# Kernel tuning notes

Measured on AMD Instinct MI355X. Metric: run time of the kernel, lower is better.

The kernel has to match this reference:

```python
import jax, jax.numpy as jnp
import numpy as np

D_MODEL = 256
NHEAD = 8
NLAYERS = 4
B, L, K = 8, 4096, 10
EPS_ATT = 1e-6
EPS_LN = 1e-5
EPS_COS = 1e-8


def setup_inputs() -> dict:
    key = jax.random.key(0)
    ks = jax.random.split(key, 12)
    s = 1.0 / np.sqrt(D_MODEL)
    s2 = 1.0 / np.sqrt(2 * D_MODEL)
    return {
        "ClassNum": K,
        "feat": jax.random.normal(ks[0], (B, L, D_MODEL), jnp.float32),
        "feat_class": jax.random.normal(ks[1], (B, K, D_MODEL), jnp.float32),
        "Wq": jax.random.normal(ks[2], (NLAYERS, D_MODEL, D_MODEL), jnp.float32) * s,
        "Wk": jax.random.normal(ks[3], (NLAYERS, D_MODEL, D_MODEL), jnp.float32) * s,
        "Wv": jax.random.normal(ks[4], (NLAYERS, D_MODEL, D_MODEL), jnp.float32) * s,
        "Wm": jax.random.normal(ks[5], (NLAYERS, D_MODEL, D_MODEL), jnp.float32) * s,
        "W1": jax.random.normal(ks[6], (NLAYERS, 2 * D_MODEL, 2 * D_MODEL), jnp.float32) * s2,
        "W2": jax.random.normal(ks[7], (NLAYERS, 2 * D_MODEL, D_MODEL), jnp.float32) * s2,
        "g1": jnp.ones((NLAYERS, D_MODEL), jnp.float32),
        "b1": jnp.zeros((NLAYERS, D_MODEL), jnp.float32),
        "g2": jnp.ones((NLAYERS, D_MODEL), jnp.float32),
        "b2": jnp.zeros((NLAYERS, D_MODEL), jnp.float32),
    }


def _layernorm(x, g, b):
    mu = jnp.mean(x, axis=-1, keepdims=True)
    xc = x - mu
    var = jnp.mean(xc * xc, axis=-1, keepdims=True)
    return g * xc * jax.lax.rsqrt(var + EPS_LN) + b


def _encoder_layer(x, oh, Wq, Wk, Wv, Wm, W1, W2, g1, b1, g2, b2):
    # x: [B,L,C], oh: [B,L,K] one-hot cluster assignment.
    # Per-cluster LoFTR linear self-attention via segment sums (exact: the
    # per-cluster v_length scaling in LinearAttention cancels algebraically).
    bsz, seq, cdim = x.shape
    hd = cdim // NHEAD
    q = (x @ Wq).reshape(bsz, seq, NHEAD, hd)
    k = (x @ Wk).reshape(bsz, seq, NHEAD, hd)
    v = (x @ Wv).reshape(bsz, seq, NHEAD, hd)
    Q = jax.nn.elu(q) + 1.0
    Kf = jax.nn.elu(k) + 1.0
    # per-(batch,cluster) sums: KV [B,K,H,D,D], Ksum [B,K,H,D]
    KV = jnp.einsum('blc,blhd,blhe->bchde', oh, Kf, v)
    Ksum = jnp.einsum('blc,blhd->bchd', oh, Kf)
    Kt = jnp.einsum('blc,bchd->blhd', oh, Ksum)  # cluster ΣK gathered per token
    Z = 1.0 / (jnp.einsum('blhd,blhd->blh', Q, Kt) + EPS_ATT)
    msg = jnp.zeros((bsz, seq, NHEAD, hd), x.dtype)
    for c in range(oh.shape[-1]):  # small fixed ClassNum loop
        msg = msg + oh[:, :, c][:, :, None, None] * jnp.einsum(
            'blhd,bhde->blhe', Q, KV[:, c])
    msg = msg * Z[..., None]
    m = msg.reshape(bsz, seq, cdim) @ Wm
    m = _layernorm(m, g1, b1)
    h = jnp.concatenate([x, m], axis=-1) @ W1
    h = jax.nn.relu(h) @ W2
    m = _layernorm(h, g2, b2)
    return x + m


def reference(ClassNum, feat, feat_class, Wq, Wk, Wv, Wm, W1, W2, g1, b1, g2, b2):
    x = jax.lax.stop_gradient(feat)          # feat.clone().detach()
    fc = jax.lax.stop_gradient(feat_class)   # feat_class.clone().detach()
    # cosine-similarity top-1 cluster routing (torch.F.cosine_similarity, eps=1e-8)
    na = jnp.linalg.norm(fc, axis=-1)  # [B,K]
    nb = jnp.linalg.norm(x, axis=-1)   # [B,L]
    dot = jnp.einsum('bkc,blc->bkl', fc, x)
    sim = dot / jnp.maximum(na[:, :, None] * nb[:, None, :], EPS_COS)
    seg = jnp.argmax(sim, axis=1)  # [B,L] cluster id per token
    oh = jax.nn.one_hot(seg, ClassNum, dtype=x.dtype)
    for li in range(Wq.shape[0]):
        x = _encoder_layer(x, oh, Wq[li], Wk[li], Wv[li], Wm[li],
                           W1[li], W2[li], g1[li], b1[li], g2[li], b2[li])
    return x
```

## Files before the change

kernel.cpp:

```cpp
#include <hip/hip_runtime.h>
#include <hip/hip_bf16.h>
#include <math.h>

#define DM 256
#define NHEAD 8
#define HD 32
#define NL 4
#define BATCH 8
#define SEQ 4096
#define KCLS 10
#define M_TOK (BATCH*SEQ)

#define BKG 64

#define PADPOS 5120
#define NWIN (PADPOS/64)
#define KVWIN 20
#define NGRP (KVWIN*4)

using bf16x8 = __attribute__((ext_vector_type(8))) short;
using f32x4  = __attribute__((ext_vector_type(4))) float;

__device__ __forceinline__ unsigned short f2bf(float f) {
    __hip_bfloat16 b = __float2bfloat16(f);
    return __builtin_bit_cast(unsigned short, b);
}
__device__ __forceinline__ float bf2f(unsigned short u) {
    unsigned v = (unsigned)u << 16;
    return __builtin_bit_cast(float, v);
}

__device__ __forceinline__ float wave_reduce_sum(float v) {
    #pragma unroll
    for (int off = 32; off > 0; off >>= 1) v += __shfl_xor(v, off, 64);
    return v;
}

__global__ __launch_bounds__(64) void fcn_kernel(const float* __restrict__ fc,
                                                 float* __restrict__ fcn) {
    int bk = blockIdx.x;
    int lane = threadIdx.x;
    float4 fv = *(const float4*)(fc + (size_t)bk * DM + lane * 4);
    float n = fv.x*fv.x + fv.y*fv.y + fv.z*fv.z + fv.w*fv.w;
    n = wave_reduce_sum(n);
    if (lane == 0) fcn[bk] = sqrtf(n);
}

__global__ void route_kernel(const float* __restrict__ feat, const float* __restrict__ fc,
                             const float* __restrict__ fcn,
                             float* __restrict__ x, unsigned short* __restrict__ xm,
                             int* __restrict__ seg) {
    int wid = (int)((blockIdx.x * (size_t)blockDim.x + threadIdx.x) >> 6);
    int lane = threadIdx.x & 63;
    if (wid >= M_TOK) return;
    int b = wid / SEQ;
    float4 xv = *(const float4*)(feat + (size_t)wid * DM + lane * 4);
    *(float4*)(x + (size_t)wid * DM + lane * 4) = xv;
    ushort4 u; u.x = f2bf(xv.x); u.y = f2bf(xv.y); u.z = f2bf(xv.z); u.w = f2bf(xv.w);
    *(ushort4*)(xm + (size_t)wid * 512 + lane * 4) = u;
    float nb2 = xv.x*xv.x + xv.y*xv.y + xv.z*xv.z + xv.w*xv.w;
    nb2 = wave_reduce_sum(nb2);
    float nb = sqrtf(nb2);
    float best = -1e30f; int bestk = 0;
    for (int k = 0; k < KCLS; ++k) {
        float4 fv = *(const float4*)(fc + ((size_t)(b * KCLS + k)) * DM + lane * 4);
        float d = fv.x*xv.x + fv.y*xv.y + fv.z*xv.z + fv.w*xv.w;
        d = wave_reduce_sum(d);
        float sim = d / fmaxf(fcn[b * KCLS + k] * nb, 1e-8f);
        if (sim > best) { best = sim; bestk = k; }
    }
    if (lane == 0) seg[wid] = bestk;
}

__global__ __launch_bounds__(256) void seg_count(const int* __restrict__ seg,
                                                 int* __restrict__ cnt) {
    __shared__ int wc[4][KCLS];
    int b = blockIdx.x >> 4, chunk = blockIdx.x & 15;
    int t = threadIdx.x, w = t >> 6, lane = t & 63;
    int c = seg[b * SEQ + chunk * 256 + t];
    #pragma unroll
    for (int cc = 0; cc < KCLS; ++cc) {
        unsigned long long m = __ballot(c == cc);
        if (lane == 0) wc[w][cc] = __popcll(m);
    }
    __syncthreads();
    if (t < KCLS)
        cnt[(b * 16 + chunk) * KCLS + t] = wc[0][t] + wc[1][t] + wc[2][t] + wc[3][t];
}

__global__ __launch_bounds__(256) void seg_scan(const int* __restrict__ cnt,
                                                int* __restrict__ chunkbase,
                                                int* __restrict__ wseg,
                                                int* __restrict__ psegp,
                                                int* __restrict__ grange) {
    __shared__ int sTot[BATCH][KCLS];
    __shared__ int sBase[BATCH][KCLS];
    int tid = threadIdx.x;
    if (tid < BATCH * KCLS) {
        int b = tid / KCLS, c = tid % KCLS;
        int run = 0;
        #pragma unroll
        for (int j = 0; j < 16; ++j) run += cnt[(b * 16 + j) * KCLS + c];
        sTot[b][c] = run;
    }
    __syncthreads();
    if (tid < BATCH) {
        int b = tid, pb = 0;
        for (int c = 0; c < KCLS; ++c) {
            sBase[b][c] = pb;
            int psz = (sTot[b][c] + 63) & ~63;
            grange[(b * KCLS + c) * 2]     = pb >> 6;
            grange[(b * KCLS + c) * 2 + 1] = (pb + psz) >> 6;
            int w0 = pb >> 6, w1 = (pb + psz) >> 6;
            for (int w = w0; w < w1; ++w) wseg[b * NWIN + w] = c;
            pb += psz;
        }
        for (int w = pb >> 6; w < NWIN; ++w) wseg[b * NWIN + w] = -1;
    }
    __syncthreads();
    for (int i = tid; i < BATCH * PADPOS; i += 256) {
        int b = i / PADPOS, pos = i % PADPOS;
        int c = KCLS - 1;
        #pragma unroll
        for (int cc = KCLS - 1; cc >= 1; --cc)
            if (pos < sBase[b][cc]) c = cc - 1;
        psegp[i] = c;
    }
    if (tid < BATCH * KCLS) {
        int b = tid / KCLS, c = tid % KCLS;
        int pre = 0;
        #pragma unroll
        for (int j = 0; j < 16; ++j) {
            chunkbase[(b * 16 + j) * KCLS + c] = sBase[b][c] + pre;
            pre += cnt[(b * 16 + j) * KCLS + c];
        }
    }
}

__global__ __launch_bounds__(256) void seg_scatter(const int* __restrict__ seg,
                                                   const int* __restrict__ chunkbase,
                                                   int* __restrict__ pidxp,
                                                   int* __restrict__ sortposG) {
    __shared__ int wc[4][KCLS];
    int b = blockIdx.x >> 4, chunk = blockIdx.x & 15;
    int t = threadIdx.x, w = t >> 6, lane = t & 63;
    int l = chunk * 256 + t;
    int c = seg[b * SEQ + l];
    int rank_w = 0;
    #pragma unroll
    for (int cc = 0; cc < KCLS; ++cc) {
        unsigned long long m = __ballot(c == cc);
        if (lane == 0) wc[w][cc] = __popcll(m);
        if (cc == c) rank_w = __popcll(m & ((1ULL << lane) - 1ULL));
    }
    __syncthreads();
    int rank = rank_w;
    for (int wp = 0; wp < 4; ++wp)
        if (wp < w) rank += wc[wp][c];
    int pos = chunkbase[(b * 16 + chunk) * KCLS + c] + rank;
    pidxp[b * PADPOS + pos] = l;
    sortposG[b * SEQ + l] = b * PADPOS + pos;
}

__global__ __launch_bounds__(256) void zero_pads(const int* __restrict__ pidxp,
                                                 unsigned short* __restrict__ Kb,
                                                 unsigned short* __restrict__ Vb) {
    int row = blockIdx.x * 8 + (threadIdx.x >> 5);
    int c8 = (threadIdx.x & 31) * 8;
    if (pidxp[row] >= 0) return;
    bf16x8 z = (bf16x8){0,0,0,0,0,0,0,0};
    *(bf16x8*)(Kb + (size_t)row * DM + c8) = z;
    *(bf16x8*)(Vb + (size_t)row * DM + c8) = z;
}

__global__ __launch_bounds__(256) void transpose_all(
    const float* __restrict__ Wq, const float* __restrict__ Wk,
    const float* __restrict__ Wv, const float* __restrict__ Wm,
    const float* __restrict__ W1, const float* __restrict__ W2,
    unsigned short* __restrict__ WqkvT, unsigned short* __restrict__ WmT,
    unsigned short* __restrict__ W1T, unsigned short* __restrict__ W2T)
{
    __shared__ float s[64][65];
    int bid = blockIdx.x;
    int li = bid / 160, r = bid % 160;
    const float* src; unsigned short* dst; int K, N, kx, ny;
    if (r < 64) {
        int which = r >> 4, idx = r & 15;
        K = 256; N = 256; kx = idx & 3; ny = idx >> 2;
        if (which == 0)      { src = Wq + (size_t)li*65536; dst = WqkvT + (size_t)li*768*256; }
        else if (which == 1) { src = Wk + (size_t)li*65536; dst = WqkvT + (size_t)li*768*256 + 65536; }
        else if (which == 2) { src = Wv + (size_t)li*65536; dst = WqkvT + (size_t)li*768*256 + 131072; }
        else                 { src = Wm + (size_t)li*65536; dst = WmT + (size_t)li*65536; }
    } else if (r < 128) {
        int idx = r - 64;
        K = 512; N = 512; kx = idx & 7; ny = idx >> 3;
        src = W1 + (size_t)li*262144; dst = W1T + (size_t)li*262144;
    } else {
        int idx = r - 128;
        K = 512; N = 256; kx = idx & 7; ny = idx >> 3;
        src = W2 + (size_t)li*131072; dst = W2T + (size_t)li*131072;
    }
    int k0 = kx * 64, n0 = ny * 64;
    int t = threadIdx.x;
    int rr = t >> 4, c4 = (t & 15) * 4;
    #pragma unroll
    for (int i = 0; i < 4; ++i) {
        float4 v = *(const float4*)(src + (size_t)(k0 + rr + i*16) * N + n0 + c4);
        s[c4+0][rr+i*16] = v.x; s[c4+1][rr+i*16] = v.y;
        s[c4+2][rr+i*16] = v.z; s[c4+3][rr+i*16] = v.w;
    }
    __syncthreads();
    #pragma unroll
    for (int i = 0; i < 4; ++i) {
        int nr = rr + i*16;
        ushort4 u;
        u.x = f2bf(s[nr][c4+0]); u.y = f2bf(s[nr][c4+1]);
        u.z = f2bf(s[nr][c4+2]); u.w = f2bf(s[nr][c4+3]);
        *(ushort4*)(dst + (size_t)(n0 + nr) * K + k0 + c4) = u;
    }
}

template<int KD, int AS, int MODE>
__global__ __launch_bounds__(512, 4) void mfma_gemm(
    const unsigned short* __restrict__ A, const unsigned short* __restrict__ Bt,
    const int* __restrict__ sortpos,
    unsigned short* __restrict__ Ob0, unsigned short* __restrict__ Ob1,
    unsigned short* __restrict__ Ob2)
{
    __shared__ unsigned short As[128 * BKG];
    __shared__ unsigned short Bs[256 * BKG];
    __shared__ int sPos[128];
    int t = threadIdx.x;
    int lane = t & 63;
    int w = t >> 6;
    int wm = w & 1, wn = w >> 1;
    int li = lane & 15, lg = lane >> 4;
    int bm = blockIdx.x * 128;
    int bn = blockIdx.y * 256;

    if (MODE == 1 && t < 128) sPos[t] = sortpos[bm + t];

    f32x4 acc[4][4];
    #pragma unroll
    for (int m = 0; m < 4; ++m)
        #pragma unroll
        for (int n = 0; n < 4; ++n)
            acc[m][n] = (f32x4){0.f, 0.f, 0.f, 0.f};

    for (int k0 = 0; k0 < KD; k0 += BKG) {
        #pragma unroll
        for (int i = 0; i < 2; ++i) {
            int chunk = i * 512 + t;
            int row = chunk >> 3, cc = chunk & 7;
            int scc = cc ^ (row & 7);
            __builtin_amdgcn_global_load_lds(
                (const __attribute__((address_space(1))) void*)(A + (size_t)(bm + row) * AS + k0 + scc * 8),
                (__attribute__((address_space(3))) void*)((char*)As + chunk * 16), 16, 0, 0);
        }
        #pragma unroll
        for (int i = 0; i < 4; ++i) {
            int chunk = i * 512 + t;
            int row = chunk >> 3, cc = chunk & 7;
            int scc = cc ^ (row & 7);
            __builtin_amdgcn_global_load_lds(
                (const __attribute__((address_space(1))) void*)(Bt + (size_t)(bn + row) * KD + k0 + scc * 8),
                (__attribute__((address_space(3))) void*)((char*)Bs + chunk * 16), 16, 0, 0);
        }
        asm volatile("s_waitcnt vmcnt(0)");
        __syncthreads();
        #pragma unroll
        for (int kk = 0; kk < 2; ++kk) {
            int jc = kk * 4 + lg;
            bf16x8 af[4], bfr[4];
            #pragma unroll
            for (int m = 0; m < 4; ++m) {
                int R = wm*64 + m*16 + li;
                af[m] = *(const bf16x8*)((const char*)As + R * 128 + ((jc ^ (R & 7)) << 4));
            }
            #pragma unroll
            for (int n = 0; n < 4; ++n) {
                int R = wn*64 + n*16 + li;
                bfr[n] = *(const bf16x8*)((const char*)Bs + R * 128 + ((jc ^ (R & 7)) << 4));
            }
            #pragma unroll
            for (int m = 0; m < 4; ++m)
                #pragma unroll
                for (int n = 0; n < 4; ++n)
                    acc[m][n] = __builtin_amdgcn_mfma_f32_16x16x32_bf16(af[m], bfr[n], acc[m][n], 0, 0, 0);
        }
        __syncthreads();
    }

    int lrow0 = wm * 64 + (lane >> 4) * 4;
    int lcol = wn * 64 + (lane & 15);
    if (MODE == 1) {
        unsigned short* Obuf = (bn < 256) ? Ob0 : (bn < 512) ? Ob1 : Ob2;
        const bool act = (bn < 512);
        #pragma unroll
        for (int m = 0; m < 4; ++m)
            #pragma unroll
            for (int n = 0; n < 4; ++n)
                #pragma unroll
                for (int j = 0; j < 4; ++j) {
                    float v = acc[m][n][j];
                    if (act) v = (v > 0.f) ? v + 1.f : expf(v);
                    int drow = sPos[lrow0 + m*16 + j];
                    Obuf[(size_t)drow * 256 + lcol + n*16] = f2bf(v);
                }
    } else {
        #pragma unroll
        for (int m = 0; m < 4; ++m)
            #pragma unroll
            for (int n = 0; n < 4; ++n)
                #pragma unroll
                for (int j = 0; j < 4; ++j)
                    Ob0[(size_t)(bm + lrow0 + m*16 + j) * 512 + bn + lcol + n*16] =
                        f2bf(fmaxf(acc[m][n][j], 0.f));
    }
}

template<int KD, int LNMODE>
__global__ __launch_bounds__(256) void gemm_ln(
    const unsigned short* __restrict__ A, const unsigned short* __restrict__ Bt,
    const float* __restrict__ g, const float* __restrict__ bb,
    float* __restrict__ x, unsigned short* __restrict__ xm)
{
    __shared__ unsigned short As[64 * BKG];
    __shared__ unsigned short Bs[256 * BKG];
    __shared__ float redS[4][64];
    __shared__ float redQ[4][64];
    int t = threadIdx.x;
    int lane = t & 63;
    int w = t >> 6;
    int li = lane & 15, lg = lane >> 4;
    int bm = blockIdx.x * 64;

    f32x4 acc[4][4];
    #pragma unroll
    for (int m = 0; m < 4; ++m)
        #pragma unroll
        for (int n = 0; n < 4; ++n)
            acc[m][n] = (f32x4){0.f, 0.f, 0.f, 0.f};

    for (int k0 = 0; k0 < KD; k0 += BKG) {
        #pragma unroll
        for (int i = 0; i < 2; ++i) {
            int chunk = i * 256 + t;
            int row = chunk >> 3, cc = chunk & 7;
            int scc = cc ^ (row & 7);
            __builtin_amdgcn_global_load_lds(
                (const __attribute__((address_space(1))) void*)(A + (size_t)(bm + row) * KD + k0 + scc * 8),
                (__attribute__((address_space(3))) void*)((char*)As + chunk * 16), 16, 0, 0);
        }
        #pragma unroll
        for (int i = 0; i < 8; ++i) {
            int chunk = i * 256 + t;
            int row = chunk >> 3, cc = chunk & 7;
            int scc = cc ^ (row & 7);
            __builtin_amdgcn_global_load_lds(
                (const __attribute__((address_space(1))) void*)(Bt + (size_t)row * KD + k0 + scc * 8),
                (__attribute__((address_space(3))) void*)((char*)Bs + chunk * 16), 16, 0, 0);
        }
        asm volatile("s_waitcnt vmcnt(0)");
        __syncthreads();
        #pragma unroll
        for (int kk = 0; kk < 2; ++kk) {
            int jc = kk * 4 + lg;
            bf16x8 af[4], bfr[4];
            #pragma unroll
            for (int m = 0; m < 4; ++m) {
                int R = m*16 + li;
                af[m] = *(const bf16x8*)((const char*)As + R * 128 + ((jc ^ (R & 7)) << 4));
            }
            #pragma unroll
            for (int n = 0; n < 4; ++n) {
                int R = w*64 + n*16 + li;
                bfr[n] = *(const bf16x8*)((const char*)Bs + R * 128 + ((jc ^ (R & 7)) << 4));
            }
            #pragma unroll
            for (int m = 0; m < 4; ++m)
                #pragma unroll
                for (int n = 0; n < 4; ++n)
                    acc[m][n] = __builtin_amdgcn_mfma_f32_16x16x32_bf16(af[m], bfr[n], acc[m][n], 0, 0, 0);
        }
        __syncthreads();
    }

    float vs[4][4], vq[4][4];
    #pragma unroll
    for (int m = 0; m < 4; ++m)
        #pragma unroll
        for (int j = 0; j < 4; ++j) {
            float s = 0.f, q = 0.f;
            #pragma unroll
            for (int n = 0; n < 4; ++n) {
                float v = acc[m][n][j];
                s += v; q += v * v;
            }
            #pragma unroll
            for (int msk = 1; msk < 16; msk <<= 1) {
                s += __shfl_xor(s, msk, 64);
                q += __shfl_xor(q, msk, 64);
            }
            vs[m][j] = s; vq[m][j] = q;
        }
    if (li == 0) {
        #pragma unroll
        for (int m = 0; m < 4; ++m)
            #pragma unroll
            for (int j = 0; j < 4; ++j) {
                redS[w][m*16 + lg*4 + j] = vs[m][j];
                redQ[w][m*16 + lg*4 + j] = vq[m][j];
            }
    }
    __syncthreads();

    float gv[4], bv[4];
    #pragma unroll
    for (int n = 0; n < 4; ++n) {
        int col = w*64 + n*16 + li;
        gv[n] = g[col]; bv[n] = bb[col];
    }
    #pragma unroll
    for (int m = 0; m < 4; ++m)
        #pragma unroll
        for (int j = 0; j < 4; ++j) {
            int r = m*16 + lg*4 + j;
            float S = redS[0][r] + redS[1][r] + redS[2][r] + redS[3][r];
            float Q = redQ[0][r] + redQ[1][r] + redQ[2][r] + redQ[3][r];
            float mu = S * (1.f / 256.f);
            float var = Q * (1.f / 256.f) - mu * mu;
            float rs = rsqrtf(var + 1e-5f);
            #pragma unroll
            for (int n = 0; n < 4; ++n) {
                int col = w*64 + n*16 + li;
                float o = gv[n] * (acc[m][n][j] - mu) * rs + bv[n];
                if (LNMODE == 1) {
                    xm[(size_t)(bm + r) * 512 + 256 + col] = f2bf(o);
                } else {
                    size_t idx = (size_t)(bm + r) * 256 + col;
                    float xv = x[idx] + o;
                    x[idx] = xv;
                    xm[(size_t)(bm + r) * 512 + col] = f2bf(xv);
                }
            }
        }
}

__global__ __launch_bounds__(256) void kv_kernel(
    const unsigned short* __restrict__ Ksrt, const unsigned short* __restrict__ Vsrt,
    float* __restrict__ part)
{
    __shared__ float sK[64 * 33];
    __shared__ float sV[64 * 33];
    int blk = blockIdx.x;
    int s = blk % KVWIN;
    int bh = blk / KVWIN;
    int b = bh >> 3, h = bh & 7;
    int t = threadIdx.x;
    int d = t >> 3, e0 = (t & 7) * 4;
    int srow = t >> 2, soff = (t & 3) * 8;
    const size_t rowbase = (size_t)(b * PADPOS + s * 256);
    float* pball = part + ((size_t)bh * NGRP + s * 4) * 1056;

    for (int g = 0; g < 4; ++g) {
        size_t gsrc = (rowbase + g * 64 + srow) * DM + h * HD + soff;
        bf16x8 k8 = *(const bf16x8*)(Ksrt + gsrc);
        bf16x8 v8 = *(const bf16x8*)(Vsrt + gsrc);
        float4 ka, kb, va, vb;
        ka.x = bf2f((unsigned short)k8[0]); ka.y = bf2f((unsigned short)k8[1]);
        ka.z = bf2f((unsigned short)k8[2]); ka.w = bf2f((unsigned short)k8[3]);
        kb.x = bf2f((unsigned short)k8[4]); kb.y = bf2f((unsigned short)k8[5]);
        kb.z = bf2f((unsigned short)k8[6]); kb.w = bf2f((unsigned short)k8[7]);
        va.x = bf2f((unsigned short)v8[0]); va.y = bf2f((unsigned short)v8[1]);
        va.z = bf2f((unsigned short)v8[2]); va.w = bf2f((unsigned short)v8[3]);
        vb.x = bf2f((unsigned short)v8[4]); vb.y = bf2f((unsigned short)v8[5]);
        vb.z = bf2f((unsigned short)v8[6]); vb.w = bf2f((unsigned short)v8[7]);
        *(float4*)(sK + srow * 33 + soff)     = ka;
        *(float4*)(sK + srow * 33 + soff + 4) = kb;
        *(float4*)(sV + srow * 33 + soff)     = va;
        *(float4*)(sV + srow * 33 + soff + 4) = vb;
        __syncthreads();

        float4 a = {0.f, 0.f, 0.f, 0.f};
        float ks = 0.f;
        #pragma unroll 8
        for (int l = 0; l < 64; ++l) {
            float kd = sK[l * 33 + d];
            float4 v4 = *(const float4*)(sV + l * 33 + e0);
            a.x = fmaf(kd, v4.x, a.x);
            a.y = fmaf(kd, v4.y, a.y);
            a.z = fmaf(kd, v4.z, a.z);
            a.w = fmaf(kd, v4.w, a.w);
            ks += kd;
        }
        float* pb = pball + g * 1056;
        *(float4*)(pb + d * 32 + e0) = a;
        if ((t & 7) == 0) pb[1024 + d] = ks;
        __syncthreads();
    }
}

__global__ __launch_bounds__(256) void kv_reduce(
    const float* __restrict__ part, const int* __restrict__ grange,
    float* __restrict__ KV, float* __restrict__ Ks)
{
    int blk = blockIdx.x;
    int c = blk % KCLS;
    int bh = blk / KCLS;
    int b = bh >> 3, h = bh & 7;
    int t = threadIdx.x;
    const float* pb = part + (size_t)bh * NGRP * 1056;
    int g0 = grange[(b * KCLS + c) * 2];
    int g1 = grange[(b * KCLS + c) * 2 + 1];
    float4 acc = {0, 0, 0, 0};
    float ka = 0.f;
    for (int gg = g0; gg < g1; ++gg) {
        float4 v = *(const float4*)(pb + (size_t)gg * 1056 + t * 4);
        acc.x += v.x; acc.y += v.y; acc.z += v.z; acc.w += v.w;
        if (t < 32) ka += pb[(size_t)gg * 1056 + 1024 + t];
    }
    *(float4*)(KV + ((size_t)(b * KCLS + c) * NHEAD + h) * HD * HD + t * 4) = acc;
    if (t < 32) Ks[((size_t)(b * KCLS + c) * NHEAD + h) * HD + t] = ka;
}

__global__ __launch_bounds__(256) void msg_kernel(
    const unsigned short* __restrict__ Qs, const float* __restrict__ KV,
    const float* __restrict__ Ks, const int* __restrict__ pidxp,
    const int* __restrict__ wseg, unsigned short* __restrict__ msgb)
{
    int b = blockIdx.x / NWIN, w = blockIdx.x % NWIN;
    int c = wseg[b * NWIN + w];
    if (c < 0) return;
    __shared__ unsigned short sQ[64 * DM];
    __shared__ unsigned short kvT[NHEAD * HD * HD];
    __shared__ float sKs[NHEAD * HD];
    __shared__ float zl[64 * NHEAD];
    __shared__ int sTok[64];
    int t = threadIdx.x;
    int wv = t >> 6, lane = t & 63;

    if (t < 64) sTok[t] = pidxp[b * PADPOS + w * 64 + t];
    { int h = t >> 5, d = t & 31;
      sKs[h * HD + d] = Ks[((size_t)(b * KCLS + c) * NHEAD + h) * HD + d]; }
    const float* kvsrc = KV + (size_t)(b * KCLS + c) * NHEAD * HD * HD;
    #pragma unroll
    for (int i = 0; i < 8; ++i) {
        int q = i * 256 + t;
        float4 v = ((const float4*)kvsrc)[q];
        int g = q * 4;
        int h = g >> 10, rem = g & 1023;
        int d = rem >> 5, e = rem & 31;
        kvT[h * 1024 + (e + 0) * 32 + d] = f2bf(v.x);
        kvT[h * 1024 + (e + 1) * 32 + d] = f2bf(v.y);
        kvT[h * 1024 + (e + 2) * 32 + d] = f2bf(v.z);
        kvT[h * 1024 + (e + 3) * 32 + d] = f2bf(v.w);
    }
    const unsigned short* qsrc = Qs + (size_t)(b * PADPOS + w * 64) * DM;
    #pragma unroll
    for (int i = 0; i < 8; ++i) {
        int q = i * 256 + t;
        *(bf16x8*)(sQ + q * 8) = *(const bf16x8*)(qsrc + q * 8);
    }
    __syncthreads();

    #pragma unroll
    for (int i = 0; i < 2; ++i) {
        int idx = i * 256 + t;
        int r = idx >> 3, h = idx & 7;
        float z = 0.f;
        #pragma unroll
        for (int d8 = 0; d8 < 4; ++d8) {
            bf16x8 qv = *(const bf16x8*)(sQ + r * DM + h * 32 + d8 * 8);
            #pragma unroll
            for (int j = 0; j < 8; ++j)
                z = fmaf(bf2f((unsigned short)qv[j]), sKs[h * HD + d8 * 8 + j], z);
        }
        zl[r * NHEAD + h] = z;
    }
    __syncthreads();

    int li = lane & 15, lg = lane >> 4;
    #pragma unroll
    for (int hh = 0; hh < 2; ++hh) {
        int h = wv * 2 + hh;
        f32x4 acc[4][2];
        #pragma unroll
        for (int m = 0; m < 4; ++m)
            #pragma unroll
            for (int n = 0; n < 2; ++n)
                acc[m][n] = (f32x4){0.f, 0.f, 0.f, 0.f};
        bf16x8 bfr[2];
        #pragma unroll
        for (int n = 0; n < 2; ++n)
            bfr[n] = *(const bf16x8*)(kvT + h * 1024 + (n * 16 + li) * 32 + lg * 8);
        #pragma unroll
        for (int m = 0; m < 4; ++m) {
            bf16x8 af = *(const bf16x8*)(sQ + (m * 16 + li) * DM + h * 32 + lg * 8);
            #pragma unroll
            for (int n = 0; n < 2; ++n)
                acc[m][n] = __builtin_amdgcn_mfma_f32_16x16x32_bf16(af, bfr[n], acc[m][n], 0, 0, 0);
        }
        #pragma unroll
        for (int m = 0; m < 4; ++m)
            #pragma unroll
            for (int n = 0; n < 2; ++n)
                #pragma unroll
                for (int j = 0; j < 4; ++j) {
                    int r = m * 16 + lg * 4 + j;
                    int tok = sTok[r];
                    if (tok >= 0) {
                        float o = acc[m][n][j] / (zl[r * NHEAD + h] + 1e-6f);
                        msgb[(size_t)(b * SEQ + tok) * DM + h * 32 + n * 16 + li] = f2bf(o);
                    }
                }
    }
}

extern "C" void kernel_launch(void* const* d_in, const int* in_sizes, int n_in,
                              void* d_out, int out_size, void* d_ws, size_t ws_size,
                              hipStream_t stream)
{
    const float* feat = (const float*)d_in[1];
    const float* fc   = (const float*)d_in[2];
    const float* Wq   = (const float*)d_in[3];
    const float* Wk   = (const float*)d_in[4];
    const float* Wv   = (const float*)d_in[5];
    const float* Wm   = (const float*)d_in[6];
    const float* W1   = (const float*)d_in[7];
    const float* W2   = (const float*)d_in[8];
    const float* g1   = (const float*)d_in[9];
    const float* b1   = (const float*)d_in[10];
    const float* g2   = (const float*)d_in[11];
    const float* b2   = (const float*)d_in[12];
    float* x = (float*)d_out;

    char* ws = (char*)d_ws;
    auto alloc = [&](size_t bytes) { char* p = ws; ws += (bytes + 255) & ~(size_t)255; return p; };
    int*   seg    = (int*)  alloc((size_t)M_TOK * 4);
    int*   cnt    = (int*)  alloc((size_t)BATCH * 16 * KCLS * 4);
    int*   cbase  = (int*)  alloc((size_t)BATCH * 16 * KCLS * 4);
    int*   pidxp  = (int*)  alloc((size_t)BATCH * PADPOS * 4);
    int*   psegp  = (int*)  alloc((size_t)BATCH * PADPOS * 4);
    int*   sortposG = (int*)alloc((size_t)M_TOK * 4);
    int*   wseg   = (int*)  alloc((size_t)BATCH * NWIN * 4);
    int*   grange = (int*)  alloc((size_t)BATCH * KCLS * 2 * 4);
    float* fcn    = (float*)alloc((size_t)BATCH * KCLS * 4);
    float* KV     = (float*)alloc((size_t)BATCH * KCLS * NHEAD * HD * HD * 4);
    float* Ks     = (float*)alloc((size_t)BATCH * KCLS * NHEAD * HD * 4);
    unsigned short* xm = (unsigned short*)alloc((size_t)M_TOK * 512 * 2);
    char* bufA = alloc((size_t)M_TOK * 512 * 2);
    unsigned short* Qs   = (unsigned short*)alloc((size_t)BATCH * PADPOS * DM * 2);
    unsigned short* Ksrt = (unsigned short*)alloc((size_t)BATCH * PADPOS * DM * 2);
    unsigned short* Vsrt = (unsigned short*)alloc((size_t)BATCH * PADPOS * DM * 2);
    unsigned short* WqkvT = (unsigned short*)alloc((size_t)NL * 768 * 256 * 2);
    unsigned short* WmT   = (unsigned short*)alloc((size_t)NL * 256 * 256 * 2);
    unsigned short* W1T   = (unsigned short*)alloc((size_t)NL * 512 * 512 * 2);
    unsigned short* W2T   = (unsigned short*)alloc((size_t)NL * 256 * 512 * 2);

    unsigned short* hb   = (unsigned short*)bufA;
    unsigned short* msgb = (unsigned short*)bufA;
    float*          part = (float*)bufA;

    transpose_all<<<NL * 160, 256, 0, stream>>>(Wq, Wk, Wv, Wm, W1, W2,
                                                WqkvT, WmT, W1T, W2T);

    fcn_kernel<<<BATCH * KCLS, 64, 0, stream>>>(fc, fcn);
    route_kernel<<<8192, 256, 0, stream>>>(feat, fc, fcn, x, xm, seg);

    seg_count<<<BATCH * 16, 256, 0, stream>>>(seg, cnt);
    seg_scan<<<1, 256, 0, stream>>>(cnt, cbase, wseg, psegp, grange);
    hipMemsetAsync(pidxp, 0xFF, (size_t)BATCH * PADPOS * 4, stream);
    seg_scatter<<<BATCH * 16, 256, 0, stream>>>(seg, cbase, pidxp, sortposG);
    zero_pads<<<BATCH * PADPOS / 8, 256, 0, stream>>>(pidxp, Ksrt, Vsrt);

    for (int li = 0; li < NL; ++li) {
        const unsigned short* wqkv = WqkvT + (size_t)li * 768 * 256;
        const unsigned short* wm   = WmT + (size_t)li * 65536;
        const unsigned short* w1   = W1T + (size_t)li * 262144;
        const unsigned short* w2   = W2T + (size_t)li * 131072;

        mfma_gemm<256, 512, 1><<<dim3(256, 3), 512, 0, stream>>>(xm, wqkv, sortposG, Qs, Ksrt, Vsrt);

        kv_kernel<<<BATCH * NHEAD * KVWIN, 256, 0, stream>>>(Ksrt, Vsrt, part);
        kv_reduce<<<BATCH * NHEAD * KCLS, 256, 0, stream>>>(part, grange, KV, Ks);

        msg_kernel<<<BATCH * NWIN, 256, 0, stream>>>(Qs, KV, Ks, pidxp, wseg, msgb);

        gemm_ln<256, 1><<<512, 256, 0, stream>>>(msgb, wm, g1 + li * DM, b1 + li * DM, nullptr, xm);

        mfma_gemm<512, 512, 2><<<dim3(256, 2), 512, 0, stream>>>(xm, w1, nullptr, hb, nullptr, nullptr);

        gemm_ln<512, 2><<<512, 256, 0, stream>>>(hb, w2, g2 + li * DM, b2 + li * DM, x, xm);
    }
}
```

Measured before the change: 650.0 us.

## Rework routing per token group, fold pad setup into scan, swap GEMM grid order

The routing kernel now handles four tokens per wave, with a 16-lane reduction per token instead of a full-wave reduction. The pidxp memset is folded into seg_scan, and zero_pads now touches only each cluster's known padding rows, found through a new prange table, instead of checking every padded row. The GEMM grid is transposed so blocks sharing an M tile run next to each other, which should improve L2 reuse of the activation tile. Together these cut launch and reduction overhead in the preprocessing kernels and change the block order of the main GEMMs.

```diff
diff --git a/kernel.cpp b/kernel.cpp
--- a/kernel.cpp
+++ b/kernel.cpp
@@ -46,30 +46,48 @@
     if (lane == 0) fcn[bk] = sqrtf(n);
 }
 
-__global__ void route_kernel(const float* __restrict__ feat, const float* __restrict__ fc,
-                             const float* __restrict__ fcn,
-                             float* __restrict__ x, unsigned short* __restrict__ xm,
-                             int* __restrict__ seg) {
-    int wid = (int)((blockIdx.x * (size_t)blockDim.x + threadIdx.x) >> 6);
-    int lane = threadIdx.x & 63;
-    if (wid >= M_TOK) return;
+__global__ __launch_bounds__(256) void route_kernel(
+    const float* __restrict__ feat, const float* __restrict__ fc,
+    const float* __restrict__ fcn,
+    float* __restrict__ x, unsigned short* __restrict__ xm,
+    int* __restrict__ seg) {
+    int t = threadIdx.x;
+    int w = t >> 6, lane = t & 63;
+    int sub = lane >> 4, sl = lane & 15;
+    int wid = blockIdx.x * 16 + w * 4 + sub;
     int b = wid / SEQ;
-    float4 xv = *(const float4*)(feat + (size_t)wid * DM + lane * 4);
-    *(float4*)(x + (size_t)wid * DM + lane * 4) = xv;
-    ushort4 u; u.x = f2bf(xv.x); u.y = f2bf(xv.y); u.z = f2bf(xv.z); u.w = f2bf(xv.w);
-    *(ushort4*)(xm + (size_t)wid * 512 + lane * 4) = u;
-    float nb2 = xv.x*xv.x + xv.y*xv.y + xv.z*xv.z + xv.w*xv.w;
-    nb2 = wave_reduce_sum(nb2);
+    float4 xv[4];
+    #pragma unroll
+    for (int i = 0; i < 4; ++i) {
+        xv[i] = *(const float4*)(feat + (size_t)wid * DM + sl * 16 + i * 4);
+        *(float4*)(x + (size_t)wid * DM + sl * 16 + i * 4) = xv[i];
+        ushort4 u;
+        u.x = f2bf(xv[i].x); u.y = f2bf(xv[i].y);
+        u.z = f2bf(xv[i].z); u.w = f2bf(xv[i].w);
+        *(ushort4*)(xm + (size_t)wid * 512 + sl * 16 + i * 4) = u;
+    }
+    float nb2 = 0.f;
+    #pragma unroll
+    for (int i = 0; i < 4; ++i)
+        nb2 += xv[i].x*xv[i].x + xv[i].y*xv[i].y + xv[i].z*xv[i].z + xv[i].w*xv[i].w;
+    #pragma unroll
+    for (int off = 1; off < 16; off <<= 1) nb2 += __shfl_xor(nb2, off, 64);
     float nb = sqrtf(nb2);
     float best = -1e30f; int bestk = 0;
     for (int k = 0; k < KCLS; ++k) {
-        float4 fv = *(const float4*)(fc + ((size_t)(b * KCLS + k)) * DM + lane * 4);
-        float d = fv.x*xv.x + fv.y*xv.y + fv.z*xv.z + fv.w*xv.w;
-        d = wave_reduce_sum(d);
+        const float* fcp = fc + ((size_t)(b * KCLS + k)) * DM + sl * 16;
+        float d = 0.f;
+        #pragma unroll
+        for (int i = 0; i < 4; ++i) {
+            float4 fv = *(const float4*)(fcp + i * 4);
+            d += fv.x*xv[i].x + fv.y*xv[i].y + fv.z*xv[i].z + fv.w*xv[i].w;
+        }
+        #pragma unroll
+        for (int off = 1; off < 16; off <<= 1) d += __shfl_xor(d, off, 64);
         float sim = d / fmaxf(fcn[b * KCLS + k] * nb, 1e-8f);
         if (sim > best) { best = sim; bestk = k; }
     }
-    if (lane == 0) seg[wid] = bestk;
+    if (sl == 0) seg[wid] = bestk;
 }
 
 __global__ __launch_bounds__(256) void seg_count(const int* __restrict__ seg,
@@ -92,7 +110,9 @@
                                                 int* __restrict__ chunkbase,
                                                 int* __restrict__ wseg,
                                                 int* __restrict__ psegp,
-                                                int* __restrict__ grange) {
+                                                int* __restrict__ grange,
+                                                int* __restrict__ prange,
+                                                int* __restrict__ pidxp) {
     __shared__ int sTot[BATCH][KCLS];
     __shared__ int sBase[BATCH][KCLS];
     int tid = threadIdx.x;
@@ -111,6 +131,8 @@
             int psz = (sTot[b][c] + 63) & ~63;
             grange[(b * KCLS + c) * 2]     = pb >> 6;
             grange[(b * KCLS + c) * 2 + 1] = (pb + psz) >> 6;
+            prange[(b * KCLS + c) * 2]     = pb + sTot[b][c];
+            prange[(b * KCLS + c) * 2 + 1] = pb + psz;
             int w0 = pb >> 6, w1 = (pb + psz) >> 6;
             for (int w = w0; w < w1; ++w) wseg[b * NWIN + w] = c;
             pb += psz;
@@ -125,6 +147,7 @@
         for (int cc = KCLS - 1; cc >= 1; --cc)
             if (pos < sBase[b][cc]) c = cc - 1;
         psegp[i] = c;
+        pidxp[i] = -1;
     }
     if (tid < BATCH * KCLS) {
         int b = tid / KCLS, c = tid % KCLS;
@@ -162,15 +185,21 @@
     sortposG[b * SEQ + l] = b * PADPOS + pos;
 }
 
-__global__ __launch_bounds__(256) void zero_pads(const int* __restrict__ pidxp,
+__global__ __launch_bounds__(256) void zero_pads(const int* __restrict__ prange,
                                                  unsigned short* __restrict__ Kb,
                                                  unsigned short* __restrict__ Vb) {
-    int row = blockIdx.x * 8 + (threadIdx.x >> 5);
-    int c8 = (threadIdx.x & 31) * 8;
-    if (pidxp[row] >= 0) return;
+    int bc = blockIdx.x;
+    int b = bc / KCLS;
+    int ps = prange[bc * 2], pe = prange[bc * 2 + 1];
+    int nrows = pe - ps;
+    int t = threadIdx.x;
     bf16x8 z = (bf16x8){0,0,0,0,0,0,0,0};
-    *(bf16x8*)(Kb + (size_t)row * DM + c8) = z;
-    *(bf16x8*)(Vb + (size_t)row * DM + c8) = z;
+    for (int idx = t; idx < nrows * 32; idx += 256) {
+        int r = idx >> 5, c8 = (idx & 31) * 8;
+        size_t row = (size_t)b * PADPOS + ps + r;
+        *(bf16x8*)(Kb + row * DM + c8) = z;
+        *(bf16x8*)(Vb + row * DM + c8) = z;
+    }
 }
 
 __global__ __launch_bounds__(256) void transpose_all(
@@ -235,8 +264,8 @@
     int w = t >> 6;
     int wm = w & 1, wn = w >> 1;
     int li = lane & 15, lg = lane >> 4;
-    int bm = blockIdx.x * 128;
-    int bn = blockIdx.y * 256;
+    int bm = blockIdx.y * 128;
+    int bn = blockIdx.x * 256;
 
     if (MODE == 1 && t < 128) sPos[t] = sortpos[bm + t];
 
@@ -645,6 +674,7 @@
     int*   sortposG = (int*)alloc((size_t)M_TOK * 4);
     int*   wseg   = (int*)  alloc((size_t)BATCH * NWIN * 4);
     int*   grange = (int*)  alloc((size_t)BATCH * KCLS * 2 * 4);
+    int*   prange = (int*)  alloc((size_t)BATCH * KCLS * 2 * 4);
     float* fcn    = (float*)alloc((size_t)BATCH * KCLS * 4);
     float* KV     = (float*)alloc((size_t)BATCH * KCLS * NHEAD * HD * HD * 4);
     float* Ks     = (float*)alloc((size_t)BATCH * KCLS * NHEAD * HD * 4);
@@ -666,13 +696,12 @@
                                                 WqkvT, WmT, W1T, W2T);
 
     fcn_kernel<<<BATCH * KCLS, 64, 0, stream>>>(fc, fcn);
-    route_kernel<<<8192, 256, 0, stream>>>(feat, fc, fcn, x, xm, seg);
+    route_kernel<<<M_TOK / 16, 256, 0, stream>>>(feat, fc, fcn, x, xm, seg);
 
     seg_count<<<BATCH * 16, 256, 0, stream>>>(seg, cnt);
-    seg_scan<<<1, 256, 0, stream>>>(cnt, cbase, wseg, psegp, grange);
-    hipMemsetAsync(pidxp, 0xFF, (size_t)BATCH * PADPOS * 4, stream);
+    seg_scan<<<1, 256, 0, stream>>>(cnt, cbase, wseg, psegp, grange, prange, pidxp);
     seg_scatter<<<BATCH * 16, 256, 0, stream>>>(seg, cbase, pidxp, sortposG);
-    zero_pads<<<BATCH * PADPOS / 8, 256, 0, stream>>>(pidxp, Ksrt, Vsrt);
+    zero_pads<<<BATCH * KCLS, 256, 0, stream>>>(prange, Ksrt, Vsrt);
 
     for (int li = 0; li < NL; ++li) {
         const unsigned short* wqkv = WqkvT + (size_t)li * 768 * 256;
@@ -680,7 +709,7 @@
         const unsigned short* w1   = W1T + (size_t)li * 262144;
         const unsigned short* w2   = W2T + (size_t)li * 131072;
 
-        mfma_gemm<256, 512, 1><<<dim3(256, 3), 512, 0, stream>>>(xm, wqkv, sortposG, Qs, Ksrt, Vsrt);
+        mfma_gemm<256, 512, 1><<<dim3(3, 256), 512, 0, stream>>>(xm, wqkv, sortposG, Qs, Ksrt, Vsrt);
 
         kv_kernel<<<BATCH * NHEAD * KVWIN, 256, 0, stream>>>(Ksrt, Vsrt, part);
         kv_reduce<<<BATCH * NHEAD * KCLS, 256, 0, stream>>>(part, grange, KV, Ks);
@@ -689,7 +718,7 @@
 
         gemm_ln<256, 1><<<512, 256, 0, stream>>>(msgb, wm, g1 + li * DM, b1 + li * DM, nullptr, xm);
 
-        mfma_gemm<512, 512, 2><<<dim3(256, 2), 512, 0, stream>>>(xm, w1, nullptr, hb, nullptr, nullptr);
+        mfma_gemm<512, 512, 2><<<dim3(2, 256), 512, 0, stream>>>(xm, w1, nullptr, hb, nullptr, nullptr);
 
         gemm_ln<512, 2><<<512, 256, 0, stream>>>(hb, w2, g2 + li * DM, b2 + li * DM, x, xm);
     }
```

Measured after the change: 675.0 us. 3.8% more time.
